# Optimization experiments

Hardware: AMD Instinct MI355X
Metric: run time of the kernel (lower is better)

## Reference

```python
import jax, jax.numpy as jnp
import numpy as np

B, L, D, H, K = 4, 2048, 1024, 16, 256
DH = D // H
SCALE = DH ** -0.5


def setup_inputs() -> dict:
    key = jax.random.key(0)
    ks = jax.random.split(key, 8)
    std = 1.0 / np.sqrt(D)
    pstd = 1.0 / np.sqrt(K)  # init_ uses last dim of (seq_len, k) tensor
    return {
        "x": jax.random.normal(ks[0], (B, L, D), dtype=jnp.float32),
        "Wq": jax.random.uniform(ks[1], (D, D), jnp.float32, -std, std),
        "Wk": jax.random.uniform(ks[2], (D, D), jnp.float32, -std, std),
        "Wv": jax.random.uniform(ks[3], (D, D), jnp.float32, -std, std),
        "proj_k": jax.random.uniform(ks[4], (L, K), jnp.float32, -pstd, pstd),
        "proj_v": jax.random.uniform(ks[5], (L, K), jnp.float32, -pstd, pstd),
        "Wo": jax.random.uniform(ks[6], (D, D), jnp.float32, -std, std),
        "bo": jax.random.uniform(ks[7], (D,), jnp.float32, -std, std),
    }


def reference(x, Wq, Wk, Wv, proj_k, proj_v, Wo, bo):
    b, l, d = x.shape
    q = x @ Wq.T                                   # [B,L,D]
    keys = jnp.einsum("bnd,nk->bkd", x @ Wk.T, proj_k)   # [B,K,D]
    vals = jnp.einsum("bnd,nk->bkd", x @ Wv.T, proj_v)   # [B,K,D]
    # faithful to original: plain reshape (B,h,L,d_h), NOT transpose-split
    q = q.reshape(b, H, l, DH)
    k = keys.reshape(b, K, H, DH).transpose(0, 2, 1, 3)  # [B,H,K,DH]
    v = vals.reshape(b, K, H, DH).transpose(0, 2, 1, 3)  # [B,H,K,DH]
    attn = jax.nn.softmax(jnp.einsum("bhld,bhkd->bhlk", q, k) * SCALE, axis=-1)
    out = jnp.einsum("bhlk,bhkd->bhld", attn, v)
    out = out.transpose(0, 2, 1, 3).reshape(b, l, d)
    return out @ Wo.T + bo
```

## Files before the change

### kernel.cpp

```cpp
#include <hip/hip_runtime.h>


typedef __attribute__((ext_vector_type(8))) short short8;
typedef __attribute__((ext_vector_type(4))) short short4_t;
typedef __attribute__((ext_vector_type(4))) float facc;

#define B_    4
#define L_    2048
#define D_    1024
#define H_    16
#define KP    256
#define DH_   64
#define SCALE_ 0.125f

__device__ __forceinline__ short f2b(float f) {
  unsigned u = __float_as_uint(f);
  unsigned r = (u + 0x7fffu + ((u >> 16) & 1u)) >> 16;
  return (short)r;
}

__device__ __forceinline__ void load16_to_lds(const short* gp, short* lp) {
  __builtin_amdgcn_global_load_lds(
      (const __attribute__((address_space(1))) void*)gp,
      (__attribute__((address_space(3))) void*)lp, 16, 0, 0);
}

__global__ __launch_bounds__(256) void prepX(
    const float* __restrict__ x,  const float* __restrict__ pk,
    const float* __restrict__ pv, const float* __restrict__ w0,
    const float* __restrict__ w1, const float* __restrict__ w2,
    const float* __restrict__ w3, short* __restrict__ xb,
    short* __restrict__ xTb, short* __restrict__ projT,
    short* __restrict__ Wb)
{
  const int z = blockIdx.z, tid = threadIdx.x;
  if (z >= 6) {
    const int bid  = blockIdx.y * 32 + blockIdx.x;
    const int widx = (z - 6) * 2 + (bid >> 10);
    const float* s = (widx == 0) ? w0 : (widx == 1) ? w1 : (widx == 2) ? w2 : w3;
    const int i = ((bid & 1023) * 256 + tid) * 4;
    float4 f = *(const float4*)(s + i);
    short4_t v; v[0] = f2b(f.x); v[1] = f2b(f.y); v[2] = f2b(f.z); v[3] = f2b(f.w);
    *(short4_t*)(Wb + (size_t)widx * 1048576 + i) = v;
    return;
  }

  __shared__ float tl[32][37];
  const int row = tid >> 3, c4 = tid & 7;

  if (z < 4) {
    const int b = z, l0 = blockIdx.y * 32, d0 = blockIdx.x * 32;
    const float* s = x + (size_t)b * L_ * D_;
    float4 f = *(const float4*)(s + (size_t)(l0 + row) * D_ + d0 + c4 * 4);
    short4_t v; v[0] = f2b(f.x); v[1] = f2b(f.y); v[2] = f2b(f.z); v[3] = f2b(f.w);
    *(short4_t*)(xb + (size_t)b * L_ * D_ + (size_t)(l0 + row) * D_ + d0 + c4 * 4) = v;
    tl[row][c4 * 4 + 0] = f.x; tl[row][c4 * 4 + 1] = f.y;
    tl[row][c4 * 4 + 2] = f.z; tl[row][c4 * 4 + 3] = f.w;
    __syncthreads();
    short4_t t;
#pragma unroll
    for (int j = 0; j < 4; j++) t[j] = f2b(tl[c4 * 4 + j][row]);
    *(short4_t*)(xTb + (size_t)b * D_ * L_ + (size_t)(d0 + row) * L_ + l0 + c4 * 4) = t;
  } else {
    if (blockIdx.x >= 8) return;
    const int sel = z - 4, l0 = blockIdx.y * 32, k0 = blockIdx.x * 32;
    const float* s = sel ? pv : pk;
    float4 f = *(const float4*)(s + (size_t)(l0 + row) * KP + k0 + c4 * 4);
    tl[row][c4 * 4 + 0] = f.x; tl[row][c4 * 4 + 1] = f.y;
    tl[row][c4 * 4 + 2] = f.z; tl[row][c4 * 4 + 3] = f.w;
    __syncthreads();
    short4_t t;
#pragma unroll
    for (int j = 0; j < 4; j++) t[j] = f2b(tl[c4 * 4 + j][row]);
    *(short4_t*)(projT + (size_t)sel * (KP * L_) + (size_t)(k0 + row) * L_ + l0 + c4 * 4) = t;
  }
}

template<int TM, int TN, int NC, bool SWZ>
__global__ __launch_bounds__(256) void gemm_lds(
    const short* __restrict__ Am, const short* __restrict__ Bm,
    const float* __restrict__ bias, float* __restrict__ C32,
    short* __restrict__ Cb, short* __restrict__ CbT, int M, int N, int K,
    long aHi, long aLo, long bHi, long bLo, long cHi, long cLo, int zDiv)
{
  constexpr int MT = TM / 32, NT = TN / 32;
  __shared__ __attribute__((aligned(16))) short As[NC][TM * 32];
  __shared__ __attribute__((aligned(16))) short Bs[NC][TN * 32];
  const int t = threadIdx.x, lane = t & 63, w = t >> 6;
  const int lm = lane & 15, g = lane >> 4;
  const int z = blockIdx.z, zhi = z / zDiv, zlo = z % zDiv;
  int bm, bn;
  if (SWZ) {
    const int p = blockIdx.y * 8 + blockIdx.x;
    bn = (p >> 3) & 7;
    bm = ((p >> 6) << 3) | (p & 7);
  } else {
    bm = blockIdx.y; bn = blockIdx.x;
  }
  const int m0 = bm * TM, n0 = bn * TN;
  const int wm = (w & 1) * (TM / 2), wn = (w >> 1) * (TN / 2);

  const short* Ab = Am + zhi * aHi + zlo * aLo;
  const short* Bp = Bm + zhi * bHi + zlo * bLo;

  facc acc[MT][NT];
  const facc fz = {0.f, 0.f, 0.f, 0.f};
#pragma unroll
  for (int i = 0; i < MT; i++)
#pragma unroll
    for (int j = 0; j < NT; j++) acc[i][j] = fz;

  const int lrow = lane >> 2;
  const int lch  = (lane & 3) * 8;

  for (int k0 = 0; k0 < K; k0 += 32 * NC) {
    __syncthreads();
#pragma unroll
    for (int c = 0; c < NC; c++) {
#pragma unroll
      for (int rnd = 0; rnd < TM / 64; rnd++) {
        const int row = rnd * 64 + w * 16;
        load16_to_lds(Ab + (size_t)(m0 + row + lrow) * K + k0 + c * 32 + lch,
                      &As[c][row * 32]);
      }
#pragma unroll
      for (int rnd = 0; rnd < TN / 64; rnd++) {
        const int row = rnd * 64 + w * 16;
        load16_to_lds(Bp + (size_t)(n0 + row + lrow) * K + k0 + c * 32 + lch,
                      &Bs[c][row * 32]);
      }
    }
    __syncthreads();

#pragma unroll
    for (int c = 0; c < NC; c++) {
      short8 af[MT], bf[NT];
#pragma unroll
      for (int mt = 0; mt < MT; mt++)
        af[mt] = *(const short8*)(&As[c][(wm + 16 * mt + lm) * 32 + g * 8]);
#pragma unroll
      for (int nt = 0; nt < NT; nt++)
        bf[nt] = *(const short8*)(&Bs[c][(wn + 16 * nt + lm) * 32 + g * 8]);
#pragma unroll
      for (int mt = 0; mt < MT; mt++)
#pragma unroll
        for (int nt = 0; nt < NT; nt++)
          acc[mt][nt] = __builtin_amdgcn_mfma_f32_16x16x32_bf16(af[mt], bf[nt], acc[mt][nt], 0, 0, 0);
    }
  }

  if (CbT && zhi == 1) {
#pragma unroll
    for (int mt = 0; mt < MT; mt++) {
      const int rb = m0 + wm + 16 * mt + 4 * g;
      const size_t bb = (size_t)(rb >> 8) * (16 * 64 * 256);
      const int kp = rb & 255;
#pragma unroll
      for (int nt = 0; nt < NT; nt++) {
        const int col = n0 + wn + 16 * nt + lm;
        short4_t o4;
#pragma unroll
        for (int r = 0; r < 4; r++) o4[r] = f2b(acc[mt][nt][r]);
        *(short4_t*)(CbT + bb + (size_t)col * KP + kp) = o4;
      }
    }
    return;
  }

  const long cz = zhi * cHi + zlo * cLo;
#pragma unroll
  for (int mt = 0; mt < MT; mt++)
#pragma unroll
    for (int r = 0; r < 4; r++) {
      const int row = m0 + wm + 16 * mt + 4 * g + r;
#pragma unroll
      for (int nt = 0; nt < NT; nt++) {
        const int col = n0 + wn + 16 * nt + lm;
        float v = acc[mt][nt][r];
        if (bias) v += bias[col];
        if (C32) C32[cz + (size_t)row * N + col] = v;
        if (Cb)  Cb[cz + (size_t)row * N + col] = f2b(v);
      }
    }
}

__global__ __launch_bounds__(256) void attn_mfma(
    const short* __restrict__ xqb, const short* __restrict__ keysb,
    const short* __restrict__ vTb, short* __restrict__ out2b)
{
  __shared__ __attribute__((aligned(16))) short Kt[2][64 * 72];
  __shared__ __attribute__((aligned(16))) short Vt[2][64 * 72];
  __shared__ __attribute__((aligned(16))) short Pt[4][32 * 72];

  const int t = threadIdx.x, lane = t & 63, w = t >> 6;
  const int lm = lane & 15, g = lane >> 4;
  const int b = blockIdx.z, h = blockIdx.y;
  const int l0w = blockIdx.x * 128 + w * 32;

  short8 aq[2][2];
#pragma unroll
  for (int mt = 0; mt < 2; mt++) {
    const int l = l0w + 16 * mt + lm;
    const short* qrow = xqb + ((size_t)b * L_ + h * 128 + (l >> 4)) * D_ + (l & 15) * DH_;
#pragma unroll
    for (int ks = 0; ks < 2; ks++)
      aq[mt][ks] = *(const short8*)(qrow + ks * 32 + g * 8);
  }

  facc accO[2][4];
  const facc fz = {0.f, 0.f, 0.f, 0.f};
#pragma unroll
  for (int mt = 0; mt < 2; mt++)
#pragma unroll
    for (int dt = 0; dt < 4; dt++) accO[mt][dt] = fz;
  float lrow[2][4];
#pragma unroll
  for (int mt = 0; mt < 2; mt++)
#pragma unroll
    for (int r = 0; r < 4; r++) lrow[mt][r] = 0.f;

  const short* Kb = keysb + (size_t)b * KP * D_ + h * DH_;
  const short* Vb = vTb + ((size_t)b * H_ + h) * DH_ * KP;

  const int srow = t >> 3, sch = (t & 7) * 8;

#pragma unroll
  for (int i = 0; i < 2; i++) {
    const int row = srow + 32 * i;
    *(short8*)(&Kt[0][row * 72 + sch]) = *(const short8*)(Kb + (size_t)row * D_ + sch);
    *(short8*)(&Vt[0][row * 72 + sch]) = *(const short8*)(Vb + (size_t)row * KP + sch);
  }
  __syncthreads();

  for (int c = 0; c < 4; c++) {
    const int bi = c & 1;
    if (c < 3) {
#pragma unroll
      for (int i = 0; i < 2; i++) {
        const int row = srow + 32 * i;
        *(short8*)(&Kt[bi ^ 1][row * 72 + sch]) =
            *(const short8*)(Kb + (size_t)((c + 1) * 64 + row) * D_ + sch);
        *(short8*)(&Vt[bi ^ 1][row * 72 + sch]) =
            *(const short8*)(Vb + (size_t)row * KP + (c + 1) * 64 + sch);
      }
    }

    facc S[2][4];
#pragma unroll
    for (int mt = 0; mt < 2; mt++)
#pragma unroll
      for (int nt = 0; nt < 4; nt++) S[mt][nt] = fz;
#pragma unroll
    for (int ks = 0; ks < 2; ks++) {
      short8 bk[4];
#pragma unroll
      for (int nt = 0; nt < 4; nt++)
        bk[nt] = *(const short8*)(&Kt[bi][(16 * nt + lm) * 72 + ks * 32 + g * 8]);
#pragma unroll
      for (int mt = 0; mt < 2; mt++)
#pragma unroll
        for (int nt = 0; nt < 4; nt++)
          S[mt][nt] = __builtin_amdgcn_mfma_f32_16x16x32_bf16(aq[mt][ks], bk[nt], S[mt][nt], 0, 0, 0);
    }

#pragma unroll
    for (int mt = 0; mt < 2; mt++)
#pragma unroll
      for (int r = 0; r < 4; r++) {
        float ps = 0.f;
        const int prow = (16 * mt + 4 * g + r) * 72;
#pragma unroll
        for (int nt = 0; nt < 4; nt++) {
          const float p = __expf(S[mt][nt][r] * SCALE_);
          ps += p;
          Pt[w][prow + 16 * nt + lm] = f2b(p);
        }
        lrow[mt][r] += ps;
      }

#pragma unroll
    for (int ks = 0; ks < 2; ks++) {
      short8 ap[2], bv[4];
#pragma unroll
      for (int mt = 0; mt < 2; mt++)
        ap[mt] = *(const short8*)(&Pt[w][(16 * mt + lm) * 72 + ks * 32 + g * 8]);
#pragma unroll
      for (int dt = 0; dt < 4; dt++)
        bv[dt] = *(const short8*)(&Vt[bi][(16 * dt + lm) * 72 + ks * 32 + g * 8]);
#pragma unroll
      for (int mt = 0; mt < 2; mt++)
#pragma unroll
        for (int dt = 0; dt < 4; dt++)
          accO[mt][dt] = __builtin_amdgcn_mfma_f32_16x16x32_bf16(ap[mt], bv[dt], accO[mt][dt], 0, 0, 0);
    }
    __syncthreads();
  }

#pragma unroll
  for (int mt = 0; mt < 2; mt++)
#pragma unroll
    for (int r = 0; r < 4; r++) {
      float ls = lrow[mt][r];
      ls += __shfl_xor(ls, 1);
      ls += __shfl_xor(ls, 2);
      ls += __shfl_xor(ls, 4);
      ls += __shfl_xor(ls, 8);
      const float inv = 1.0f / ls;
      const int l = l0w + 16 * mt + 4 * g + r;
#pragma unroll
      for (int dt = 0; dt < 4; dt++)
        out2b[((size_t)b * L_ + l) * D_ + h * DH_ + 16 * dt + lm] = f2b(accO[mt][dt][r] * inv);
    }
}

extern "C" void kernel_launch(void* const* d_in, const int* in_sizes, int n_in,
                              void* d_out, int out_size, void* d_ws, size_t ws_size,
                              hipStream_t stream)
{
  const float* x      = (const float*)d_in[0];
  const float* Wq     = (const float*)d_in[1];
  const float* Wk     = (const float*)d_in[2];
  const float* Wv     = (const float*)d_in[3];
  const float* proj_k = (const float*)d_in[4];
  const float* proj_v = (const float*)d_in[5];
  const float* Wo     = (const float*)d_in[6];
  const float* bo     = (const float*)d_in[7];
  float* out = (float*)d_out;

  short* ws     = (short*)d_ws;
  short* xqb    = ws;
  short* xTb    = xqb    + 8388608;
  short* xb     = xTb    + 8388608;
  short* out2b  = xb;
  short* Wqb    = xb     + 8388608;
  short* Wkb    = Wqb    + 1048576;
  short* Wvb    = Wkb    + 1048576;
  short* Wob    = Wvb    + 1048576;
  short* projTk = Wob    + 1048576;
  short* projTv = projTk + 524288;
  short* xk2b   = projTv + 524288;
  short* xv2b   = xk2b   + 1048576;
  short* keysb  = xv2b   + 1048576;
  short* valsb  = keysb  + 1048576;
  short* vT     = valsb  + 1048576;
  (void)Wkb; (void)Wvb; (void)projTv; (void)xv2b; (void)valsb;

  prepX<<<dim3(32, 64, 8), 256, 0, stream>>>(
      x, proj_k, proj_v, Wq, Wk, Wv, Wo, xb, xTb, projTk, Wqb);

  gemm_lds<128, 128, 2, true><<<dim3(8, 64, 1), 256, 0, stream>>>(
      xb, Wqb, nullptr, nullptr, xqb, nullptr, 8192, 1024, 1024,
      0, 0, 0, 0, 0, 0, 1);

  gemm_lds<64, 64, 2, false><<<dim3(16, 4, 8), 256, 0, stream>>>(
      projTk, xTb, nullptr, nullptr, xk2b, nullptr, 256, 1024, 2048,
      524288, 0, 0, (long)D_ * L_, 1048576, 262144, 4);

  gemm_lds<64, 64, 2, false><<<dim3(16, 16, 2), 256, 0, stream>>>(
      xk2b, Wkb, nullptr, nullptr, keysb, vT, 1024, 1024, 1024,
      1048576, 0, 1048576, 0, 0, 0, 1);

  attn_mfma<<<dim3(16, 16, 4), 256, 0, stream>>>(xqb, keysb, vT, out2b);

  gemm_lds<128, 128, 2, true><<<dim3(8, 64, 1), 256, 0, stream>>>(
      out2b, Wob, bo, out, nullptr, nullptr, 8192, 1024, 1024,
      0, 0, 0, 0, 0, 0, 1);
}
```

Baseline: 232.5 us.

## Add 8-wave 256x128 triple-buffered GEMM for Q and output projections

Adds a new bf16 MFMA GEMM kernel with 512 threads, 256x128 block tiles, 64-wide K steps and a three-stage LDS ring. It issues direct global-to-LDS loads with an XOR swizzle and prefetches two stages ahead, interleaving those loads with MFMA work and raising wave priority around the MFMA section. The kernel replaces the 128x128 double-buffered GEMM for the Q projection and the final output projection. It needs 144 KB of dynamic shared memory, set once through a static flag, and the larger tiles halve the grid to 256 blocks, which may reduce occupancy or load balance.

```diff
diff --git a/kernel.cpp b/kernel.cpp
--- a/kernel.cpp
+++ b/kernel.cpp
@@ -74,6 +74,124 @@
     for (int j = 0; j < 4; j++) t[j] = f2b(tl[c4 * 4 + j][row]);
     *(short4_t*)(projT + (size_t)sel * (KP * L_) + (size_t)(k0 + row) * L_ + l0 + c4 * 4) = t;
   }
+}
+
+__global__ __launch_bounds__(512, 2) void gemm8p(
+    const short* __restrict__ Am, const short* __restrict__ Bm,
+    const float* __restrict__ bias, float* __restrict__ C32,
+    short* __restrict__ Cb, int M, int N, int K)
+{
+  extern __shared__ __attribute__((aligned(16))) short smem[];
+  constexpr int BUF  = 24576;
+  constexpr int BOFF = 16384;
+
+  const int t = threadIdx.x, lane = t & 63, w = t >> 6;
+  const int lm = lane & 15, g = lane >> 4;
+  const int bm = blockIdx.x * 4 + (blockIdx.y >> 3);
+  const int bn = blockIdx.y & 7;
+  const int m0 = bm * 256, n0 = bn * 128;
+  const int wm = (w & 3) * 64, wn = (w >> 2) * 64;
+
+  const int srow = lane >> 2;
+  const int sslot = lane & 3;
+
+  facc acc[4][4];
+  const facc fz = {0.f, 0.f, 0.f, 0.f};
+#pragma unroll
+  for (int i = 0; i < 4; i++)
+#pragma unroll
+    for (int j = 0; j < 4; j++) acc[i][j] = fz;
+
+  auto stageA = [&](int kt, int buf, int rnd) {
+    const int task = rnd * 8 + w;
+    const int c = task >> 4, grp = task & 15;
+    const int row = grp * 16 + srow;
+    const int slot = sslot ^ ((row >> 1) & 3);
+    load16_to_lds(Am + (size_t)(m0 + row) * K + kt * 64 + c * 32 + slot * 8,
+                  smem + buf * BUF + c * 8192 + grp * 512);
+  };
+  auto stageB = [&](int kt, int buf, int rnd) {
+    const int task = rnd * 8 + w;
+    const int c = task >> 3, grp = task & 7;
+    const int row = grp * 16 + srow;
+    const int slot = sslot ^ ((row >> 1) & 3);
+    load16_to_lds(Bm + (size_t)(n0 + row) * K + kt * 64 + c * 32 + slot * 8,
+                  smem + buf * BUF + BOFF + c * 4096 + grp * 512);
+  };
+
+#pragma unroll
+  for (int r = 0; r < 4; r++) stageA(0, 0, r);
+#pragma unroll
+  for (int r = 0; r < 2; r++) stageB(0, 0, r);
+#pragma unroll
+  for (int r = 0; r < 4; r++) stageA(1, 1, r);
+#pragma unroll
+  for (int r = 0; r < 2; r++) stageB(1, 1, r);
+  asm volatile("s_waitcnt vmcnt(6)" ::: "memory");
+  __builtin_amdgcn_sched_barrier(0);
+  __builtin_amdgcn_s_barrier();
+
+  const int T = K >> 6;
+  int p = 0;
+  for (int kt = 0; kt < T; kt++) {
+    const int q = (p == 0) ? 2 : p - 1;
+    const bool pf = (kt + 2 < T);
+
+#pragma unroll
+    for (int c = 0; c < 2; c++) {
+      short8 af[4], bf[4];
+      const int abase = p * BUF + c * 8192;
+      const int bbase = p * BUF + BOFF + c * 4096;
+#pragma unroll
+      for (int mt = 0; mt < 4; mt++) {
+        const int row = wm + 16 * mt + lm;
+        af[mt] = *(const short8*)(smem + abase + row * 32 + ((g ^ ((row >> 1) & 3)) * 8));
+      }
+#pragma unroll
+      for (int nt = 0; nt < 4; nt++) {
+        const int row = wn + 16 * nt + lm;
+        bf[nt] = *(const short8*)(smem + bbase + row * 32 + ((g ^ ((row >> 1) & 3)) * 8));
+      }
+      if (pf) {
+        if (c == 0) { stageA(kt + 2, q, 0); stageA(kt + 2, q, 1); stageB(kt + 2, q, 0); }
+        else        { stageA(kt + 2, q, 2); stageA(kt + 2, q, 3); stageB(kt + 2, q, 1); }
+      }
+      __builtin_amdgcn_s_barrier();
+      __builtin_amdgcn_s_setprio(1);
+#pragma unroll
+      for (int mt = 0; mt < 4; mt++)
+#pragma unroll
+        for (int nt = 0; nt < 4; nt++)
+          acc[mt][nt] = __builtin_amdgcn_mfma_f32_16x16x32_bf16(af[mt], bf[nt], acc[mt][nt], 0, 0, 0);
+      __builtin_amdgcn_s_setprio(0);
+      if (c == 0) __builtin_amdgcn_s_barrier();
+    }
+
+    if (pf) {
+      asm volatile("s_waitcnt vmcnt(6)" ::: "memory");
+      __builtin_amdgcn_sched_barrier(0);
+    } else if (kt + 1 < T) {
+      asm volatile("s_waitcnt vmcnt(0)" ::: "memory");
+      __builtin_amdgcn_sched_barrier(0);
+    }
+    __builtin_amdgcn_s_barrier();
+    p = (p == 2) ? 0 : p + 1;
+  }
+
+#pragma unroll
+  for (int mt = 0; mt < 4; mt++)
+#pragma unroll
+    for (int r = 0; r < 4; r++) {
+      const int row = m0 + wm + 16 * mt + 4 * g + r;
+#pragma unroll
+      for (int nt = 0; nt < 4; nt++) {
+        const int col = n0 + wn + 16 * nt + lm;
+        float v = acc[mt][nt][r];
+        if (bias) v += bias[col];
+        if (C32) C32[(size_t)row * N + col] = v;
+        if (Cb)  Cb[(size_t)row * N + col] = f2b(v);
+      }
+    }
 }
 
 template<int TM, int TN, int NC, bool SWZ>
@@ -345,12 +463,18 @@
   short* vT     = valsb  + 1048576;
   (void)Wkb; (void)Wvb; (void)projTv; (void)xv2b; (void)valsb;
 
+  static bool attr_set = false;
+  if (!attr_set) {
+    (void)hipFuncSetAttribute(reinterpret_cast<const void*>(gemm8p),
+                              hipFuncAttributeMaxDynamicSharedMemorySize, 147456);
+    attr_set = true;
+  }
+
   prepX<<<dim3(32, 64, 8), 256, 0, stream>>>(
       x, proj_k, proj_v, Wq, Wk, Wv, Wo, xb, xTb, projTk, Wqb);
 
-  gemm_lds<128, 128, 2, true><<<dim3(8, 64, 1), 256, 0, stream>>>(
-      xb, Wqb, nullptr, nullptr, xqb, nullptr, 8192, 1024, 1024,
-      0, 0, 0, 0, 0, 0, 1);
+  gemm8p<<<dim3(8, 32, 1), 512, 147456, stream>>>(
+      xb, Wqb, nullptr, nullptr, xqb, 8192, 1024, 1024);
 
   gemm_lds<64, 64, 2, false><<<dim3(16, 4, 8), 256, 0, stream>>>(
       projTk, xTb, nullptr, nullptr, xk2b, nullptr, 256, 1024, 2048,
@@ -362,7 +486,6 @@
 
   attn_mfma<<<dim3(16, 16, 4), 256, 0, stream>>>(xqb, keysb, vT, out2b);
 
-  gemm_lds<128, 128, 2, true><<<dim3(8, 64, 1), 256, 0, stream>>>(
-      out2b, Wob, bo, out, nullptr, nullptr, 8192, 1024, 1024,
-      0, 0, 0, 0, 0, 0, 1);
-}
+  gemm8p<<<dim3(8, 32, 1), 512, 147456, stream>>>(
+      out2b, Wob, bo, out, nullptr, 8192, 1024, 1024);
+}
```

Result: faster. 227.5 us (-2.1%).
